# Optimization experiments

Hardware: AMD Instinct MI355X
Metric: run time of the kernel (lower is better)

## Reference

```python
import jax, jax.numpy as jnp
import numpy as np

# Config mirroring MultiHeadAttention1d(in_channels=256, n_heads=8, residual=False,
# kernel_size=1, attention_type=0) applied to 3-D inputs (B, C, N).
B, C, N, H, D = 4, 256, 2048, 8, 256  # per-head dim D = in_channels; OC = H*D = 2048
OC = H * D


def setup_inputs() -> dict:
    key = jax.random.key(0)
    ks = jax.random.split(key, 14)
    s = 1.0 / np.sqrt(C)
    f32 = jnp.float32
    inp = {
        "x": jax.random.normal(ks[0], (B, C, N), f32),
        "y": jax.random.normal(ks[1], (B, C, N), f32),
        # ConvNormActivation1d (kernel_size=1) == pointwise conv + (folded, eval-mode)
        # BatchNorm affine + ReLU. BN folds to per-channel scale g and shift beta.
        "Wq": jax.random.normal(ks[2], (OC, C), f32) * s,
        "bq": jax.random.normal(ks[3], (OC,), f32) * 0.01,
        "gq": jnp.ones((OC,), f32),
        "betaq": jnp.zeros((OC,), f32),
        "Wk": jax.random.normal(ks[4], (OC, C), f32) * s,
        "bk": jax.random.normal(ks[5], (OC,), f32) * 0.01,
        "gk": jnp.ones((OC,), f32),
        "betak": jnp.zeros((OC,), f32),
        "Wv": jax.random.normal(ks[6], (OC, C), f32) * s,
        "bv": jax.random.normal(ks[7], (OC,), f32) * 0.01,
        "gv": jnp.ones((OC,), f32),
        "betav": jnp.zeros((OC,), f32),
    }
    return inp


def _cna(W, b, g, beta, t):
    # 1x1 conv (channel GEMM) + folded-BN affine + ReLU; t: (B, C, N) -> (B, OC, N)
    z = jnp.einsum("oc,bcn->bon", W, t) + b[:, None]
    return jax.nn.relu(g[:, None] * z + beta[:, None])


def _heads(t):
    # (B, OC, N) -> (B, H, N, D); channel split matches torch.split chunks of size D
    return t.reshape(B, H, D, N).transpose(0, 1, 3, 2)


def reference(x, y, Wq, bq, gq, betaq, Wk, bk, gk, betak, Wv, bv, gv, betav):
    q = _heads(_cna(Wq, bq, gq, betaq, x))  # (B,H,N,D)
    k = _heads(_cna(Wk, bk, gk, betak, y))
    v = _heads(_cna(Wv, bv, gv, betav, y))
    energy = jnp.einsum("bhnd,bhmd->bhnm", q, k)  # bmm(Q, K^T)
    attn = jax.nn.softmax(energy, axis=-1)
    out = jnp.einsum("bhnm,bhmd->bhnd", attn, v)  # (B,H,N,D)
    # torch path: view(H,B,k,N,D).permute(1,0,3,2,4) -> (B,H,N,k=1,D);
    # squeeze(dim=2) is a no-op since N != 1.
    return out[:, :, :, None, :]  # (B, H, N, 1, D)
```

## Files before the change

### kernel.cpp

```cpp
#include <hip/hip_runtime.h>
#include <cstdint>
#include <cstddef>

typedef unsigned short u16;
typedef __attribute__((ext_vector_type(4))) float f32x4;
typedef __attribute__((ext_vector_type(16))) float f32x16;
typedef __attribute__((ext_vector_type(8))) _Float16 f16x8;
typedef __attribute__((ext_vector_type(4))) u16   u16x4;
typedef __attribute__((ext_vector_type(8))) u16   u16x8;
typedef __attribute__((ext_vector_type(4))) int   i32x4;

#define DEV static __device__ __forceinline__
#define MFMA16(a,b,c) __builtin_amdgcn_mfma_f32_16x16x32_f16((a),(b),(c),0,0,0)
#define MFMA32(a,b,c) __builtin_amdgcn_mfma_f32_32x32x16_f16((a),(b),(c),0,0,0)

constexpr int Bc = 4, Cc = 256, Nc = 2048, Hc = 8, Dc = 256, OCc = 2048;

constexpr size_t OFF_XT = 0;
constexpr size_t OFF_YT = OFF_XT + (size_t)Bc*Nc*Cc*2;
constexpr size_t OFF_WQ = OFF_YT + (size_t)Bc*Nc*Cc*2;
constexpr size_t OFF_WK = OFF_WQ + (size_t)OCc*Cc*2;
constexpr size_t OFF_WV = OFF_WK + (size_t)OCc*Cc*2;
constexpr size_t OFF_BQ = OFF_WV + (size_t)OCc*Cc*2;
constexpr size_t OFF_BK = OFF_BQ + (size_t)OCc*4;
constexpr size_t OFF_BV = OFF_BK + (size_t)OCc*4;
constexpr size_t OFF_Q  = OFF_BV + (size_t)OCc*4;
constexpr size_t OFF_K  = OFF_Q  + (size_t)Bc*Hc*Nc*Dc*2;
constexpr size_t OFF_V  = OFF_K  + (size_t)Bc*Hc*Nc*Dc*2;

DEV u16 f2h(float x){
  _Float16 h = (_Float16)x;
  return __builtin_bit_cast(u16, h);
}

DEV void load_lds16(const void* g, void* l){
  __builtin_amdgcn_global_load_lds((const __attribute__((address_space(1))) int*)g,
                                   (__attribute__((address_space(3))) int*)l, 16, 0, 0);
}

__global__ __launch_bounds__(256) void transpose_cast(const float* __restrict__ x,
                                                      const float* __restrict__ y,
                                                      u16* __restrict__ XT,
                                                      u16* __restrict__ YT){
  __shared__ u16 tile[64][65];
  int b = blockIdx.z >> 1;
  const float* src = (blockIdx.z & 1) ? y : x;
  u16* dst = (blockIdx.z & 1) ? YT : XT;
  int n0 = blockIdx.x * 64, c0 = blockIdx.y * 64;
  int t = threadIdx.x;
#pragma unroll
  for (int i = 0; i < 16; ++i){
    int slot = i*256 + t;
    int cl = slot >> 6, nl = slot & 63;
    tile[cl][nl] = f2h(src[((size_t)b*Cc + c0 + cl)*Nc + n0 + nl]);
  }
  __syncthreads();
#pragma unroll
  for (int i = 0; i < 8; ++i){
    int slot = i*256 + t;
    int nl = slot >> 5, cl = (slot & 31)*2;
    uint32_t v = (uint32_t)tile[cl][nl] | ((uint32_t)tile[cl+1][nl] << 16);
    *(uint32_t*)(dst + ((size_t)b*Nc + n0 + nl)*Cc + c0 + cl) = v;
  }
}

__global__ __launch_bounds__(256) void prep_w(const float* __restrict__ W,
                                              const float* __restrict__ bsrc,
                                              const float* __restrict__ g,
                                              const float* __restrict__ beta,
                                              u16* __restrict__ Wo,
                                              float* __restrict__ bb){
  int idx = (blockIdx.x*256 + threadIdx.x) * 8;
  int o = idx >> 8, c = idx & 255;
  float gg = g[o];
  f32x4 a0 = *(const f32x4*)(W + idx);
  f32x4 a1 = *(const f32x4*)(W + idx + 4);
  u16x8 r;
#pragma unroll
  for (int i = 0; i < 4; ++i){ r[i] = f2h(a0[i]*gg); r[i+4] = f2h(a1[i]*gg); }
  *(u16x8*)(Wo + idx) = r;
  if (c == 0) bb[o] = gg*bsrc[o] + beta[o];
}

template<int SW>
__global__ __launch_bounds__(256, 2) void proj_gemm(const u16* __restrict__ Xt,
                                                    const u16* __restrict__ Wp,
                                                    const float* __restrict__ bb,
                                                    u16* __restrict__ outp){
  __shared__ __align__(16) char lds[32768];
  int t = threadIdx.x, w = t >> 6, l = t & 63, q = l & 15, g = l >> 4;
  int b = blockIdx.z;
  int n0 = blockIdx.x * 128, o0 = blockIdx.y * 128;
  int fs = ((q >> 1) & 3) << 4;
  int partg = ((l & 3) ^ ((l >> 3) & 3));
  f32x4 acc[4][4] = {};

  for (int it = 0; it < 4; ++it){
    __syncthreads();
#pragma unroll
    for (int j = 0; j < 8; ++j){
      int s = j*4 + w;
      int chunk = s >> 3;
      int off = (s & 7) * 1024;
      int row = (s & 7)*16 + (l >> 2);
      const char* gsrc;
      if (chunk < 2)
        gsrc = (const char*)(Wp + (size_t)(o0 + row)*Cc) + it*128 + chunk*64 + partg*16;
      else
        gsrc = (const char*)(Xt + ((size_t)b*Nc + n0 + row)*Cc) + it*128 + (chunk & 1)*64 + partg*16;
      load_lds16(gsrc, lds + chunk*8192 + off);
    }
    asm volatile("s_waitcnt vmcnt(0)" ::: "memory");
    __syncthreads();
#pragma unroll
    for (int kc = 0; kc < 2; ++kc){
      f16x8 fw[4], fx[4];
#pragma unroll
      for (int i = 0; i < 4; ++i){
        int wrow = (SW ? (w & 1) : (w >> 1))*64 + i*16 + q;
        int xrow = (SW ? (w >> 1) : (w & 1))*64 + i*16 + q;
        fw[i] = *(const f16x8*)(lds + kc*8192 + wrow*64 + ((g*16) ^ fs));
        fx[i] = *(const f16x8*)(lds + 16384 + kc*8192 + xrow*64 + ((g*16) ^ fs));
      }
#pragma unroll
      for (int i = 0; i < 4; ++i)
#pragma unroll
        for (int jj = 0; jj < 4; ++jj){
          if constexpr (!SW) acc[i][jj] = MFMA16(fw[i], fx[jj], acc[i][jj]);
          else               acc[i][jj] = MFMA16(fx[i], fw[jj], acc[i][jj]);
        }
    }
  }

  if constexpr (!SW) {
    f32x4 bias[4];
#pragma unroll
    for (int i = 0; i < 4; ++i) bias[i] = *(const f32x4*)(bb + o0 + (w>>1)*64 + i*16 + 4*g);
#pragma unroll
    for (int i = 0; i < 4; ++i)
#pragma unroll
      for (int jj = 0; jj < 4; ++jj){
        u16x4 pk;
#pragma unroll
        for (int r = 0; r < 4; ++r){
          float z = acc[i][jj][r] + bias[i][r];
          pk[r] = f2h(fmaxf(z, 0.f));
        }
        int o = o0 + (w>>1)*64 + i*16 + 4*g;
        int n = n0 + (w&1)*64 + jj*16 + q;
        int hh = o >> 8, d = o & 255;
        *(u16x4*)(outp + ((size_t)((b*Hc + hh)*Nc + n))*Dc + d) = pk;
      }
  } else {
    float biasv[4];
#pragma unroll
    for (int i = 0; i < 4; ++i) biasv[i] = bb[o0 + (w&1)*64 + i*16 + q];
#pragma unroll
    for (int i = 0; i < 4; ++i)
#pragma unroll
      for (int jj = 0; jj < 4; ++jj){
        u16x4 pk;
#pragma unroll
        for (int r = 0; r < 4; ++r){
          float z = acc[i][jj][r] + biasv[jj];
          pk[r] = f2h(fmaxf(z, 0.f));
        }
        int o = o0 + (w&1)*64 + jj*16 + q;
        int n = n0 + (w>>1)*64 + i*16 + 4*g;
        int hh = o >> 8, d = o & 255;
        *(u16x4*)(outp + ((size_t)((b*Hc + hh)*Dc + d))*Nc + n) = pk;
      }
  }
}

__global__ __launch_bounds__(512, 1) void attn_kernel(const u16* __restrict__ Qp,
                                                      const u16* __restrict__ Kp,
                                                      const u16* __restrict__ Vp,
                                                      float* __restrict__ outp){
  __shared__ __align__(16) char lds[150528];
  const int t = threadIdx.x, w = t >> 6, l = t & 63, lq = l & 31, hi = l >> 5;
  const int wq = w & 3, wm = w >> 2;
  const int h = blockIdx.y, b = blockIdx.z;
  const int q0 = blockIdx.x * 128;
  size_t head = (size_t)(b*Hc + h) * Nc * Dc;
  const u16* Qh = Qp + head;
  const u16* Kh = Kp + head;
  const u16* Vh = Vp + head;

  char* Pex  = lds + 131072;
  float* smax = (float*)(lds + 147456);
  float* ssum = (float*)(lds + 148480);
  float* sscl = (float*)(lds + 149504);
  float* slinv= (float*)(lds + 150016);

  f16x8 qf[16];
  {
    const u16* qrow = Qh + (size_t)(q0 + wq*32 + lq) * Dc;
#pragma unroll
    for (int kc = 0; kc < 16; ++kc) qf[kc] = *(const f16x8*)(qrow + kc*16 + hi*8);
  }

  f32x16 acc[4] = {};
  float m_run = -1e30f, l_run = 0.f;

#define STAGE_KV(m0_, buf_)                                                        \
  {                                                                                \
    char* Kd = lds + (buf_)*32768;                                                 \
    char* Vd = lds + 65536 + (buf_)*32768;                                         \
    _Pragma("unroll")                                                              \
    for (int j = 0; j < 4; ++j){                                                   \
      int row = w*8 + j*2 + hi;                                                    \
      int gs = (l & 31) ^ (row & 7);                                               \
      load_lds16(Kh + (size_t)((m0_) + row)*Dc + gs*8, Kd + w*4096 + j*1024);      \
    }                                                                              \
    _Pragma("unroll")                                                              \
    for (int j = 0; j < 4; ++j){                                                   \
      int ri = w*4 + j;                                                            \
      int rd = ri*8 + (l >> 3);                                                    \
      int gs = (l & 7) ^ (rd & 7);                                                 \
      load_lds16(Vh + (size_t)rd*Nc + (m0_) + gs*8, Vd + ri*1024 + l*16);          \
    }                                                                              \
  }

  STAGE_KV(0, 0);
  asm volatile("s_waitcnt vmcnt(0)" ::: "memory");
  __syncthreads();

  for (int it = 0; it < 32; ++it){
    const int cur = it & 1;
    char* Kc = lds + cur*32768;
    char* Vc = lds + 65536 + cur*32768;

    if (it < 31) STAGE_KV((it + 1)*64, cur ^ 1);

    f32x16 s = {};
    __builtin_amdgcn_s_setprio(1);
#pragma unroll
    for (int kc = 0; kc < 16; ++kc){
      f16x8 kf = *(const f16x8*)(Kc + (wm*32 + lq)*512 + ((kc*32 + hi*16) ^ ((l & 7) << 4)));
      s = MFMA32(kf, qf[kc], s);
    }
    __builtin_amdgcn_s_setprio(0);

    float tmax = s[0];
#pragma unroll
    for (int r = 1; r < 16; ++r) tmax = fmaxf(tmax, s[r]);
    tmax = fmaxf(tmax, __shfl_xor(tmax, 32));
    if (!hi) smax[(wq*2 + wm)*32 + lq] = tmax;
    __syncthreads();
    float omax = smax[(wq*2 + (1 - wm))*32 + lq];
    float mnew = fmaxf(m_run, fmaxf(tmax, omax));
    float scale = __expf(m_run - mnew);

    float p[16];
    float rsum = 0.f;
#pragma unroll
    for (int r = 0; r < 16; ++r){ p[r] = __expf(s[r] - mnew); rsum += p[r]; }
    rsum += __shfl_xor(rsum, 32);
    if (!hi){
      ssum[(wq*2 + wm)*32 + lq] = rsum;
      if (!wm) sscl[wq*32 + lq] = scale;
    }

    int pk[8];
#pragma unroll
    for (int j2 = 0; j2 < 8; ++j2)
      pk[j2] = __builtin_bit_cast(int, __builtin_amdgcn_cvt_pkrtz(p[2*j2], p[2*j2+1]));
    int sx[8];
#pragma unroll
    for (int j2 = 0; j2 < 8; ++j2) sx[j2] = __shfl_xor(pk[j2], 32);
    i32x4 f0, f1;
    f0[0] = hi ? sx[2] : pk[0];  f0[1] = hi ? sx[3] : pk[1];
    f0[2] = hi ? pk[2] : sx[0];  f0[3] = hi ? pk[3] : sx[1];
    f1[0] = hi ? sx[6] : pk[4];  f1[1] = hi ? sx[7] : pk[5];
    f1[2] = hi ? pk[6] : sx[4];  f1[3] = hi ? pk[7] : sx[5];
    *(i32x4*)(Pex + w*2048 + l*16)        = f0;
    *(i32x4*)(Pex + w*2048 + 1024 + l*16) = f1;
    __syncthreads();

    float osum = ssum[(wq*2 + (1 - wm))*32 + lq];
    l_run = l_run * scale + rsum + osum;
    m_run = mnew;

    float sc[16];
#pragma unroll
    for (int r = 0; r < 16; ++r) sc[r] = sscl[wq*32 + (r & 3) + 8*(r >> 2) + 4*hi];
#pragma unroll
    for (int dt = 0; dt < 4; ++dt)
#pragma unroll
      for (int r = 0; r < 16; ++r) acc[dt][r] *= sc[r];

    i32x4 g0 = *(const i32x4*)(Pex + (w ^ 4)*2048 + l*16);
    i32x4 g1 = *(const i32x4*)(Pex + (w ^ 4)*2048 + 1024 + l*16);
    f16x8 a0 = __builtin_bit_cast(f16x8, wm ? g0 : f0);
    f16x8 a1 = __builtin_bit_cast(f16x8, wm ? g1 : f1);
    f16x8 a2 = __builtin_bit_cast(f16x8, wm ? f0 : g0);
    f16x8 a3 = __builtin_bit_cast(f16x8, wm ? f1 : g1);

    __builtin_amdgcn_s_setprio(1);
#pragma unroll
    for (int h2 = 0; h2 < 2; ++h2)
#pragma unroll
      for (int dt = 0; dt < 4; ++dt)
#pragma unroll
        for (int mcl = 0; mcl < 2; ++mcl){
          f16x8 vf = *(const f16x8*)(Vc + (wm*128 + dt*32 + lq)*128 +
                                     (((h2*4 + mcl*2 + hi)*16) ^ ((l & 7) << 4)));
          f16x8 af = h2 ? (mcl ? a3 : a2) : (mcl ? a1 : a0);
          acc[dt] = MFMA32(af, vf, acc[dt]);
        }
    __builtin_amdgcn_s_setprio(0);

    asm volatile("s_waitcnt vmcnt(0)" ::: "memory");
    __syncthreads();
  }
#undef STAGE_KV

  if (!hi && !wm) slinv[wq*32 + lq] = 1.f / l_run;
  __syncthreads();
  float li[16];
#pragma unroll
  for (int r = 0; r < 16; ++r) li[r] = slinv[wq*32 + (r & 3) + 8*(r >> 2) + 4*hi];
#pragma unroll
  for (int dt = 0; dt < 4; ++dt)
#pragma unroll
    for (int r = 0; r < 16; ++r){
      int qrow_ = wq*32 + (r & 3) + 8*(r >> 2) + 4*hi;
      int d = wm*128 + dt*32 + lq;
      outp[head + (size_t)(q0 + qrow_)*Dc + d] = acc[dt][r] * li[r];
    }
}

extern "C" void kernel_launch(void* const* d_in, const int* in_sizes, int n_in,
                              void* d_out, int out_size, void* d_ws, size_t ws_size,
                              hipStream_t stream){
  const float* x     = (const float*)d_in[0];
  const float* y     = (const float*)d_in[1];
  const float* Wq    = (const float*)d_in[2];
  const float* bq    = (const float*)d_in[3];
  const float* gq    = (const float*)d_in[4];
  const float* betaq = (const float*)d_in[5];
  const float* Wk    = (const float*)d_in[6];
  const float* bk    = (const float*)d_in[7];
  const float* gk    = (const float*)d_in[8];
  const float* betak = (const float*)d_in[9];
  const float* Wv    = (const float*)d_in[10];
  const float* bv    = (const float*)d_in[11];
  const float* gv    = (const float*)d_in[12];
  const float* betav = (const float*)d_in[13];
  char* ws = (char*)d_ws;
  float* outp = (float*)d_out;

  u16* XT = (u16*)(ws + OFF_XT);
  u16* YT = (u16*)(ws + OFF_YT);
  u16* WQb = (u16*)(ws + OFF_WQ);
  u16* WKb = (u16*)(ws + OFF_WK);
  u16* WVb = (u16*)(ws + OFF_WV);
  float* BQ = (float*)(ws + OFF_BQ);
  float* BK = (float*)(ws + OFF_BK);
  float* BV = (float*)(ws + OFF_BV);
  u16* Qw = (u16*)(ws + OFF_Q);
  u16* Kw = (u16*)(ws + OFF_K);
  u16* Vw = (u16*)(ws + OFF_V);

  transpose_cast<<<dim3(Nc/64, Cc/64, Bc*2), 256, 0, stream>>>(x, y, XT, YT);
  prep_w<<<dim3(OCc*Cc/2048), 256, 0, stream>>>(Wq, bq, gq, betaq, WQb, BQ);
  prep_w<<<dim3(OCc*Cc/2048), 256, 0, stream>>>(Wk, bk, gk, betak, WKb, BK);
  prep_w<<<dim3(OCc*Cc/2048), 256, 0, stream>>>(Wv, bv, gv, betav, WVb, BV);

  dim3 pg(Nc/128, OCc/128, Bc);
  proj_gemm<0><<<pg, 256, 0, stream>>>(XT, WQb, BQ, Qw);
  proj_gemm<0><<<pg, 256, 0, stream>>>(YT, WKb, BK, Kw);
  proj_gemm<1><<<pg, 256, 0, stream>>>(YT, WVb, BV, Vw);

  attn_kernel<<<dim3(Nc/128, Hc, Bc), 512, 0, stream>>>(Qw, Kw, Vw, outp);
}
```

Baseline: 270.8 us.

## Give each wave full key/value tiles and 32 queries, dropping cross-wave softmax exchange

The attention kernel now processes 256 queries per block, with each of the 8 waves owning 32 query rows and the full 256-wide head dimension and all 64 keys per tile. This removes the shared-memory exchange of row maxima, sums, scales and P fragments and two barriers per iteration. It also adds a lazy rescale that only updates the running max when it grows by more than 8. The cost is doubled accumulator registers (8 f32x16 per lane) and half as many blocks, which risks register spills and fewer blocks to fill the GPU.

```diff
diff --git a/kernel.cpp b/kernel.cpp
--- a/kernel.cpp
+++ b/kernel.cpp
@@ -177,30 +177,23 @@
                                                       const u16* __restrict__ Kp,
                                                       const u16* __restrict__ Vp,
                                                       float* __restrict__ outp){
-  __shared__ __align__(16) char lds[150528];
+  __shared__ __align__(16) char lds[131072];
   const int t = threadIdx.x, w = t >> 6, l = t & 63, lq = l & 31, hi = l >> 5;
-  const int wq = w & 3, wm = w >> 2;
   const int h = blockIdx.y, b = blockIdx.z;
-  const int q0 = blockIdx.x * 128;
+  const int q0 = blockIdx.x * 256;
   size_t head = (size_t)(b*Hc + h) * Nc * Dc;
   const u16* Qh = Qp + head;
   const u16* Kh = Kp + head;
   const u16* Vh = Vp + head;
 
-  char* Pex  = lds + 131072;
-  float* smax = (float*)(lds + 147456);
-  float* ssum = (float*)(lds + 148480);
-  float* sscl = (float*)(lds + 149504);
-  float* slinv= (float*)(lds + 150016);
-
   f16x8 qf[16];
   {
-    const u16* qrow = Qh + (size_t)(q0 + wq*32 + lq) * Dc;
+    const u16* qrow = Qh + (size_t)(q0 + w*32 + lq) * Dc;
 #pragma unroll
     for (int kc = 0; kc < 16; ++kc) qf[kc] = *(const f16x8*)(qrow + kc*16 + hi*8);
   }
 
-  f32x16 acc[4] = {};
+  f32x16 acc[8] = {};
   float m_run = -1e30f, l_run = 0.f;
 
 #define STAGE_KV(m0_, buf_)                                                        \
@@ -218,7 +211,7 @@
       int ri = w*4 + j;                                                            \
       int rd = ri*8 + (l >> 3);                                                    \
       int gs = (l & 7) ^ (rd & 7);                                                 \
-      load_lds16(Vh + (size_t)rd*Nc + (m0_) + gs*8, Vd + ri*1024 + l*16);          \
+      load_lds16(Vh + (size_t)rd*Nc + (m0_) + gs*8, Vd + ri*1024);                 \
     }                                                                              \
   }
 
@@ -233,82 +226,87 @@
 
     if (it < 31) STAGE_KV((it + 1)*64, cur ^ 1);
 
-    f32x16 s = {};
+    f32x16 s0 = {}, s1 = {};
     __builtin_amdgcn_s_setprio(1);
 #pragma unroll
     for (int kc = 0; kc < 16; ++kc){
-      f16x8 kf = *(const f16x8*)(Kc + (wm*32 + lq)*512 + ((kc*32 + hi*16) ^ ((l & 7) << 4)));
-      s = MFMA32(kf, qf[kc], s);
+      int off = (kc*32 + hi*16) ^ ((l & 7) << 4);
+      f16x8 kf0 = *(const f16x8*)(Kc + lq*512 + off);
+      f16x8 kf1 = *(const f16x8*)(Kc + (32 + lq)*512 + off);
+      s0 = MFMA32(kf0, qf[kc], s0);
+      s1 = MFMA32(kf1, qf[kc], s1);
     }
     __builtin_amdgcn_s_setprio(0);
 
-    float tmax = s[0];
-#pragma unroll
-    for (int r = 1; r < 16; ++r) tmax = fmaxf(tmax, s[r]);
+    float tmax = s0[0];
+#pragma unroll
+    for (int r = 1; r < 16; ++r) tmax = fmaxf(tmax, s0[r]);
+#pragma unroll
+    for (int r = 0; r < 16; ++r) tmax = fmaxf(tmax, s1[r]);
     tmax = fmaxf(tmax, __shfl_xor(tmax, 32));
-    if (!hi) smax[(wq*2 + wm)*32 + lq] = tmax;
-    __syncthreads();
-    float omax = smax[(wq*2 + (1 - wm))*32 + lq];
-    float mnew = fmaxf(m_run, fmaxf(tmax, omax));
-    float scale = __expf(m_run - mnew);
-
-    float p[16];
+
+    float meff = m_run, scale = 1.f;
+    if (!__all(tmax <= m_run + 8.f)){
+      meff = fmaxf(m_run, tmax);
+      scale = __expf(m_run - meff);
+      m_run = meff;
+#pragma unroll
+      for (int r = 0; r < 16; ++r){
+        float scr = __shfl(scale, (r & 3) + 8*(r >> 2) + 4*hi);
+#pragma unroll
+        for (int dt = 0; dt < 8; ++dt) acc[dt][r] *= scr;
+      }
+    }
+
     float rsum = 0.f;
 #pragma unroll
-    for (int r = 0; r < 16; ++r){ p[r] = __expf(s[r] - mnew); rsum += p[r]; }
+    for (int r = 0; r < 16; ++r){ s0[r] = __expf(s0[r] - meff); rsum += s0[r]; }
+#pragma unroll
+    for (int r = 0; r < 16; ++r){ s1[r] = __expf(s1[r] - meff); rsum += s1[r]; }
     rsum += __shfl_xor(rsum, 32);
-    if (!hi){
-      ssum[(wq*2 + wm)*32 + lq] = rsum;
-      if (!wm) sscl[wq*32 + lq] = scale;
-    }
-
-    int pk[8];
-#pragma unroll
-    for (int j2 = 0; j2 < 8; ++j2)
-      pk[j2] = __builtin_bit_cast(int, __builtin_amdgcn_cvt_pkrtz(p[2*j2], p[2*j2+1]));
-    int sx[8];
-#pragma unroll
-    for (int j2 = 0; j2 < 8; ++j2) sx[j2] = __shfl_xor(pk[j2], 32);
-    i32x4 f0, f1;
-    f0[0] = hi ? sx[2] : pk[0];  f0[1] = hi ? sx[3] : pk[1];
-    f0[2] = hi ? pk[2] : sx[0];  f0[3] = hi ? pk[3] : sx[1];
-    f1[0] = hi ? sx[6] : pk[4];  f1[1] = hi ? sx[7] : pk[5];
-    f1[2] = hi ? pk[6] : sx[4];  f1[3] = hi ? pk[7] : sx[5];
-    *(i32x4*)(Pex + w*2048 + l*16)        = f0;
-    *(i32x4*)(Pex + w*2048 + 1024 + l*16) = f1;
-    __syncthreads();
-
-    float osum = ssum[(wq*2 + (1 - wm))*32 + lq];
-    l_run = l_run * scale + rsum + osum;
-    m_run = mnew;
-
-    float sc[16];
-#pragma unroll
-    for (int r = 0; r < 16; ++r) sc[r] = sscl[wq*32 + (r & 3) + 8*(r >> 2) + 4*hi];
-#pragma unroll
-    for (int dt = 0; dt < 4; ++dt)
-#pragma unroll
-      for (int r = 0; r < 16; ++r) acc[dt][r] *= sc[r];
-
-    i32x4 g0 = *(const i32x4*)(Pex + (w ^ 4)*2048 + l*16);
-    i32x4 g1 = *(const i32x4*)(Pex + (w ^ 4)*2048 + 1024 + l*16);
-    f16x8 a0 = __builtin_bit_cast(f16x8, wm ? g0 : f0);
-    f16x8 a1 = __builtin_bit_cast(f16x8, wm ? g1 : f1);
-    f16x8 a2 = __builtin_bit_cast(f16x8, wm ? f0 : g0);
-    f16x8 a3 = __builtin_bit_cast(f16x8, wm ? f1 : g1);
+    l_run = l_run * scale + rsum;
+
+    f16x8 a0, a1, a2, a3;
+    {
+      int pk[8], sx[8];
+#pragma unroll
+      for (int j2 = 0; j2 < 8; ++j2)
+        pk[j2] = __builtin_bit_cast(int, __builtin_amdgcn_cvt_pkrtz(s0[2*j2], s0[2*j2+1]));
+#pragma unroll
+      for (int j2 = 0; j2 < 8; ++j2) sx[j2] = __shfl_xor(pk[j2], 32);
+      i32x4 c0, c1;
+      c0[0] = hi ? sx[2] : pk[0];  c0[1] = hi ? sx[3] : pk[1];
+      c0[2] = hi ? pk[2] : sx[0];  c0[3] = hi ? pk[3] : sx[1];
+      c1[0] = hi ? sx[6] : pk[4];  c1[1] = hi ? sx[7] : pk[5];
+      c1[2] = hi ? pk[6] : sx[4];  c1[3] = hi ? pk[7] : sx[5];
+      a0 = __builtin_bit_cast(f16x8, c0);
+      a1 = __builtin_bit_cast(f16x8, c1);
+    }
+    {
+      int pk[8], sx[8];
+#pragma unroll
+      for (int j2 = 0; j2 < 8; ++j2)
+        pk[j2] = __builtin_bit_cast(int, __builtin_amdgcn_cvt_pkrtz(s1[2*j2], s1[2*j2+1]));
+#pragma unroll
+      for (int j2 = 0; j2 < 8; ++j2) sx[j2] = __shfl_xor(pk[j2], 32);
+      i32x4 c0, c1;
+      c0[0] = hi ? sx[2] : pk[0];  c0[1] = hi ? sx[3] : pk[1];
+      c0[2] = hi ? pk[2] : sx[0];  c0[3] = hi ? pk[3] : sx[1];
+      c1[0] = hi ? sx[6] : pk[4];  c1[1] = hi ? sx[7] : pk[5];
+      c1[2] = hi ? pk[6] : sx[4];  c1[3] = hi ? pk[7] : sx[5];
+      a2 = __builtin_bit_cast(f16x8, c0);
+      a3 = __builtin_bit_cast(f16x8, c1);
+    }
 
     __builtin_amdgcn_s_setprio(1);
 #pragma unroll
-    for (int h2 = 0; h2 < 2; ++h2)
-#pragma unroll
-      for (int dt = 0; dt < 4; ++dt)
-#pragma unroll
-        for (int mcl = 0; mcl < 2; ++mcl){
-          f16x8 vf = *(const f16x8*)(Vc + (wm*128 + dt*32 + lq)*128 +
-                                     (((h2*4 + mcl*2 + hi)*16) ^ ((l & 7) << 4)));
-          f16x8 af = h2 ? (mcl ? a3 : a2) : (mcl ? a1 : a0);
-          acc[dt] = MFMA32(af, vf, acc[dt]);
-        }
+    for (int dt = 0; dt < 8; ++dt)
+#pragma unroll
+      for (int ks = 0; ks < 4; ++ks){
+        f16x8 vf = *(const f16x8*)(Vc + (dt*32 + lq)*128 + (((ks*2 + hi) ^ (l & 7)) << 4));
+        f16x8 af = (ks == 0) ? a0 : (ks == 1) ? a1 : (ks == 2) ? a2 : a3;
+        acc[dt] = MFMA32(af, vf, acc[dt]);
+      }
     __builtin_amdgcn_s_setprio(0);
 
     asm volatile("s_waitcnt vmcnt(0)" ::: "memory");
@@ -316,19 +314,16 @@
   }
 #undef STAGE_KV
 
-  if (!hi && !wm) slinv[wq*32 + lq] = 1.f / l_run;
-  __syncthreads();
-  float li[16];
-#pragma unroll
-  for (int r = 0; r < 16; ++r) li[r] = slinv[wq*32 + (r & 3) + 8*(r >> 2) + 4*hi];
-#pragma unroll
-  for (int dt = 0; dt < 4; ++dt)
-#pragma unroll
-    for (int r = 0; r < 16; ++r){
-      int qrow_ = wq*32 + (r & 3) + 8*(r >> 2) + 4*hi;
-      int d = wm*128 + dt*32 + lq;
-      outp[head + (size_t)(q0 + qrow_)*Dc + d] = acc[dt][r] * li[r];
-    }
+  float inv_own = 1.f / l_run;
+#pragma unroll
+  for (int r = 0; r < 16; ++r){
+    int qrow_ = (r & 3) + 8*(r >> 2) + 4*hi;
+    float invr = __shfl(inv_own, (r & 3) + 8*(r >> 2) + 4*hi);
+    size_t obase = head + (size_t)(q0 + w*32 + qrow_)*Dc + lq;
+#pragma unroll
+    for (int dt = 0; dt < 8; ++dt)
+      outp[obase + dt*32] = acc[dt][r] * invr;
+  }
 }
 
 extern "C" void kernel_launch(void* const* d_in, const int* in_sizes, int n_in,
@@ -373,5 +368,5 @@
   proj_gemm<0><<<pg, 256, 0, stream>>>(YT, WKb, BK, Kw);
   proj_gemm<1><<<pg, 256, 0, stream>>>(YT, WVb, BV, Vw);
 
-  attn_kernel<<<dim3(Nc/128, Hc, Bc), 512, 0, stream>>>(Qw, Kw, Vw, outp);
-}
+  attn_kernel<<<dim3(Nc/256, Hc, Bc), 512, 0, stream>>>(Qw, Kw, Vw, outp);
+}
```

New measurement: 629.3 us. 132% more time.

## Load V straight from global into registers, single-buffer K, add lazy softmax rescaling

Applied to the files above, without the earlier changes.

The attention kernel no longer stages V in LDS. Each wave loads its V fragments directly from global memory into registers in two halves, interleaved with the PV MFMAs and with the next K tile prefetch. K becomes single-buffered with a new XOR swizzle, which shrinks LDS from about 150KB to 50KB, and the launch bound is raised to allow several blocks per CU. The softmax now rescales the accumulators only when the running max grows by more than 8, sharing the per-row scale and the inverse sum by shuffle instead of through LDS. This trades LDS capacity for more global traffic and register pressure, and it risks stalls from the uncoalesced strided V reads.

```diff
diff --git a/kernel.cpp b/kernel.cpp
--- a/kernel.cpp
+++ b/kernel.cpp
@@ -173,11 +173,11 @@
   }
 }
 
-__global__ __launch_bounds__(512, 1) void attn_kernel(const u16* __restrict__ Qp,
+__global__ __launch_bounds__(512, 4) void attn_kernel(const u16* __restrict__ Qp,
                                                       const u16* __restrict__ Kp,
                                                       const u16* __restrict__ Vp,
                                                       float* __restrict__ outp){
-  __shared__ __align__(16) char lds[150528];
+  __shared__ __align__(16) char lds[51200];
   const int t = threadIdx.x, w = t >> 6, l = t & 63, lq = l & 31, hi = l >> 5;
   const int wq = w & 3, wm = w >> 2;
   const int h = blockIdx.y, b = blockIdx.z;
@@ -187,11 +187,10 @@
   const u16* Kh = Kp + head;
   const u16* Vh = Vp + head;
 
-  char* Pex  = lds + 131072;
-  float* smax = (float*)(lds + 147456);
-  float* ssum = (float*)(lds + 148480);
-  float* sscl = (float*)(lds + 149504);
-  float* slinv= (float*)(lds + 150016);
+  char* Kl  = lds;
+  char* Pex = lds + 32768;
+  float* smax = (float*)(lds + 49152);
+  float* ssum = (float*)(lds + 50176);
 
   f16x8 qf[16];
   {
@@ -202,42 +201,39 @@
 
   f32x16 acc[4] = {};
   float m_run = -1e30f, l_run = 0.f;
-
-#define STAGE_KV(m0_, buf_)                                                        \
+  const int lsw = lq ^ ((lq >> 3) & 3);
+
+#define STAGE_K(m0_)                                                               \
   {                                                                                \
-    char* Kd = lds + (buf_)*32768;                                                 \
-    char* Vd = lds + 65536 + (buf_)*32768;                                         \
     _Pragma("unroll")                                                              \
     for (int j = 0; j < 4; ++j){                                                   \
       int row = w*8 + j*2 + hi;                                                    \
-      int gs = (l & 31) ^ (row & 7);                                               \
-      load_lds16(Kh + (size_t)((m0_) + row)*Dc + gs*8, Kd + w*4096 + j*1024);      \
+      int r5 = row & 31;                                                           \
+      int gs = (l & 31) ^ r5 ^ ((r5 >> 3) & 3);                                    \
+      load_lds16(Kh + (size_t)((m0_) + row)*Dc + gs*8, Kl + w*4096 + j*1024);      \
     }                                                                              \
-    _Pragma("unroll")                                                              \
-    for (int j = 0; j < 4; ++j){                                                   \
-      int ri = w*4 + j;                                                            \
-      int rd = ri*8 + (l >> 3);                                                    \
-      int gs = (l & 7) ^ (rd & 7);                                                 \
-      load_lds16(Vh + (size_t)rd*Nc + (m0_) + gs*8, Vd + ri*1024 + l*16);          \
-    }                                                                              \
-  }
-
-  STAGE_KV(0, 0);
+  }
+
+  STAGE_K(0);
   asm volatile("s_waitcnt vmcnt(0)" ::: "memory");
   __syncthreads();
 
   for (int it = 0; it < 32; ++it){
-    const int cur = it & 1;
-    char* Kc = lds + cur*32768;
-    char* Vc = lds + 65536 + cur*32768;
-
-    if (it < 31) STAGE_KV((it + 1)*64, cur ^ 1);
+    const int m0 = it * 64;
+    const int mn = ((it < 31) ? (it + 1) : 31) * 64;
+
+    f16x8 vA[8];
+#pragma unroll
+    for (int ks = 0; ks < 2; ++ks)
+#pragma unroll
+      for (int dt = 0; dt < 4; ++dt)
+        vA[ks*4 + dt] = *(const f16x8*)(Vh + (size_t)(wm*128 + dt*32 + lq)*Nc + m0 + ks*16 + hi*8);
 
     f32x16 s = {};
     __builtin_amdgcn_s_setprio(1);
 #pragma unroll
     for (int kc = 0; kc < 16; ++kc){
-      f16x8 kf = *(const f16x8*)(Kc + (wm*32 + lq)*512 + ((kc*32 + hi*16) ^ ((l & 7) << 4)));
+      f16x8 kf = *(const f16x8*)(Kl + (wm*32 + lq)*512 + (((kc*2 + hi) ^ lsw) << 4));
       s = MFMA32(kf, qf[kc], s);
     }
     __builtin_amdgcn_s_setprio(0);
@@ -249,18 +245,27 @@
     if (!hi) smax[(wq*2 + wm)*32 + lq] = tmax;
     __syncthreads();
     float omax = smax[(wq*2 + (1 - wm))*32 + lq];
-    float mnew = fmaxf(m_run, fmaxf(tmax, omax));
-    float scale = __expf(m_run - mnew);
+    float cmax = fmaxf(tmax, omax);
+
+    float meff = m_run, scale = 1.f;
+    if (!__all(cmax <= m_run + 8.f)){
+      meff = fmaxf(m_run, cmax);
+      scale = __expf(m_run - meff);
+      m_run = meff;
+#pragma unroll
+      for (int r = 0; r < 16; ++r){
+        float scr = __shfl(scale, (r & 3) + 8*(r >> 2) + 4*hi);
+#pragma unroll
+        for (int dt = 0; dt < 4; ++dt) acc[dt][r] *= scr;
+      }
+    }
 
     float p[16];
     float rsum = 0.f;
 #pragma unroll
-    for (int r = 0; r < 16; ++r){ p[r] = __expf(s[r] - mnew); rsum += p[r]; }
+    for (int r = 0; r < 16; ++r){ p[r] = __expf(s[r] - meff); rsum += p[r]; }
     rsum += __shfl_xor(rsum, 32);
-    if (!hi){
-      ssum[(wq*2 + wm)*32 + lq] = rsum;
-      if (!wm) sscl[wq*32 + lq] = scale;
-    }
+    if (!hi) ssum[(wq*2 + wm)*32 + lq] = rsum;
 
     int pk[8];
 #pragma unroll
@@ -280,15 +285,6 @@
 
     float osum = ssum[(wq*2 + (1 - wm))*32 + lq];
     l_run = l_run * scale + rsum + osum;
-    m_run = mnew;
-
-    float sc[16];
-#pragma unroll
-    for (int r = 0; r < 16; ++r) sc[r] = sscl[wq*32 + (r & 3) + 8*(r >> 2) + 4*hi];
-#pragma unroll
-    for (int dt = 0; dt < 4; ++dt)
-#pragma unroll
-      for (int r = 0; r < 16; ++r) acc[dt][r] *= sc[r];
 
     i32x4 g0 = *(const i32x4*)(Pex + (w ^ 4)*2048 + l*16);
     i32x4 g1 = *(const i32x4*)(Pex + (w ^ 4)*2048 + 1024 + l*16);
@@ -297,38 +293,49 @@
     f16x8 a2 = __builtin_bit_cast(f16x8, wm ? f0 : g0);
     f16x8 a3 = __builtin_bit_cast(f16x8, wm ? f1 : g1);
 
+    asm volatile("s_waitcnt vmcnt(0)" ::: "memory");
     __builtin_amdgcn_s_setprio(1);
 #pragma unroll
-    for (int h2 = 0; h2 < 2; ++h2)
+    for (int dt = 0; dt < 4; ++dt){
+      acc[dt] = MFMA32(a0, vA[dt],     acc[dt]);
+      acc[dt] = MFMA32(a1, vA[4 + dt], acc[dt]);
+    }
+    __builtin_amdgcn_s_setprio(0);
+
+    f16x8 vB[8];
+#pragma unroll
+    for (int ks = 0; ks < 2; ++ks)
 #pragma unroll
       for (int dt = 0; dt < 4; ++dt)
-#pragma unroll
-        for (int mcl = 0; mcl < 2; ++mcl){
-          f16x8 vf = *(const f16x8*)(Vc + (wm*128 + dt*32 + lq)*128 +
-                                     (((h2*4 + mcl*2 + hi)*16) ^ ((l & 7) << 4)));
-          f16x8 af = h2 ? (mcl ? a3 : a2) : (mcl ? a1 : a0);
-          acc[dt] = MFMA32(af, vf, acc[dt]);
-        }
+        vB[ks*4 + dt] = *(const f16x8*)(Vh + (size_t)(wm*128 + dt*32 + lq)*Nc + m0 + 32 + ks*16 + hi*8);
+
+    STAGE_K(mn);
+
+    asm volatile("s_waitcnt vmcnt(4)" ::: "memory");
+
+    __builtin_amdgcn_s_setprio(1);
+#pragma unroll
+    for (int dt = 0; dt < 4; ++dt){
+      acc[dt] = MFMA32(a2, vB[dt],     acc[dt]);
+      acc[dt] = MFMA32(a3, vB[4 + dt], acc[dt]);
+    }
     __builtin_amdgcn_s_setprio(0);
 
     asm volatile("s_waitcnt vmcnt(0)" ::: "memory");
     __syncthreads();
   }
-#undef STAGE_KV
-
-  if (!hi && !wm) slinv[wq*32 + lq] = 1.f / l_run;
-  __syncthreads();
-  float li[16];
-#pragma unroll
-  for (int r = 0; r < 16; ++r) li[r] = slinv[wq*32 + (r & 3) + 8*(r >> 2) + 4*hi];
-#pragma unroll
-  for (int dt = 0; dt < 4; ++dt)
-#pragma unroll
-    for (int r = 0; r < 16; ++r){
-      int qrow_ = wq*32 + (r & 3) + 8*(r >> 2) + 4*hi;
-      int d = wm*128 + dt*32 + lq;
-      outp[head + (size_t)(q0 + qrow_)*Dc + d] = acc[dt][r] * li[r];
-    }
+#undef STAGE_K
+
+  float inv_own = 1.f / l_run;
+#pragma unroll
+  for (int r = 0; r < 16; ++r){
+    int crow = (r & 3) + 8*(r >> 2) + 4*hi;
+    float invr = __shfl(inv_own, crow);
+    size_t obase = head + (size_t)(q0 + wq*32 + crow)*Dc + wm*128 + lq;
+#pragma unroll
+    for (int dt = 0; dt < 4; ++dt)
+      outp[obase + dt*32] = acc[dt][r] * invr;
+  }
 }
 
 extern "C" void kernel_launch(void* const* d_in, const int* in_sizes, int n_in,
```

New measurement: 1.020 ms. 3.77x slower.

## Skip softmax rescale when max grows little, retune LDS swizzle, shuffle scales

Applied to the files above, without the earlier changes.

Adds a lazy online-softmax update: the running max and the accumulator rescale are only refreshed when some row's new max exceeds the running max by more than a threshold, checked wave-wide. Per-row scale and final 1/l are broadcast with lane shuffles instead of LDS round trips. The K tile swizzle gains an extra XOR term to cut LDS bank conflicts on reads. The V LDS destination offset drops the per-lane term, presumably because the LDS DMA load addresses per lane implicitly. The lazy max trades fewer exp and multiply passes for some risk of fp16 P overflow or precision loss if the threshold is too loose.

```diff
diff --git a/kernel.cpp b/kernel.cpp
--- a/kernel.cpp
+++ b/kernel.cpp
@@ -190,8 +190,6 @@
   char* Pex  = lds + 131072;
   float* smax = (float*)(lds + 147456);
   float* ssum = (float*)(lds + 148480);
-  float* sscl = (float*)(lds + 149504);
-  float* slinv= (float*)(lds + 150016);
 
   f16x8 qf[16];
   {
@@ -202,6 +200,7 @@
 
   f32x16 acc[4] = {};
   float m_run = -1e30f, l_run = 0.f;
+  const int lsw = lq ^ ((lq >> 3) & 3);
 
 #define STAGE_KV(m0_, buf_)                                                        \
   {                                                                                \
@@ -210,7 +209,8 @@
     _Pragma("unroll")                                                              \
     for (int j = 0; j < 4; ++j){                                                   \
       int row = w*8 + j*2 + hi;                                                    \
-      int gs = (l & 31) ^ (row & 7);                                               \
+      int r5 = row & 31;                                                           \
+      int gs = (l & 31) ^ r5 ^ ((r5 >> 3) & 3);                                    \
       load_lds16(Kh + (size_t)((m0_) + row)*Dc + gs*8, Kd + w*4096 + j*1024);      \
     }                                                                              \
     _Pragma("unroll")                                                              \
@@ -218,7 +218,7 @@
       int ri = w*4 + j;                                                            \
       int rd = ri*8 + (l >> 3);                                                    \
       int gs = (l & 7) ^ (rd & 7);                                                 \
-      load_lds16(Vh + (size_t)rd*Nc + (m0_) + gs*8, Vd + ri*1024 + l*16);          \
+      load_lds16(Vh + (size_t)rd*Nc + (m0_) + gs*8, Vd + ri*1024);                 \
     }                                                                              \
   }
 
@@ -237,7 +237,7 @@
     __builtin_amdgcn_s_setprio(1);
 #pragma unroll
     for (int kc = 0; kc < 16; ++kc){
-      f16x8 kf = *(const f16x8*)(Kc + (wm*32 + lq)*512 + ((kc*32 + hi*16) ^ ((l & 7) << 4)));
+      f16x8 kf = *(const f16x8*)(Kc + (wm*32 + lq)*512 + (((kc*2 + hi) ^ lsw) << 4));
       s = MFMA32(kf, qf[kc], s);
     }
     __builtin_amdgcn_s_setprio(0);
@@ -249,18 +249,22 @@
     if (!hi) smax[(wq*2 + wm)*32 + lq] = tmax;
     __syncthreads();
     float omax = smax[(wq*2 + (1 - wm))*32 + lq];
-    float mnew = fmaxf(m_run, fmaxf(tmax, omax));
-    float scale = __expf(m_run - mnew);
+    float cmax = fmaxf(tmax, omax);
+
+    float meff = m_run, scale = 1.f;
+    const bool need = !__all(cmax <= m_run + 8.f);
+    if (need){
+      meff = fmaxf(m_run, cmax);
+      scale = __expf(m_run - meff);
+      m_run = meff;
+    }
 
     float p[16];
     float rsum = 0.f;
 #pragma unroll
-    for (int r = 0; r < 16; ++r){ p[r] = __expf(s[r] - mnew); rsum += p[r]; }
+    for (int r = 0; r < 16; ++r){ p[r] = __expf(s[r] - meff); rsum += p[r]; }
     rsum += __shfl_xor(rsum, 32);
-    if (!hi){
-      ssum[(wq*2 + wm)*32 + lq] = rsum;
-      if (!wm) sscl[wq*32 + lq] = scale;
-    }
+    if (!hi) ssum[(wq*2 + wm)*32 + lq] = rsum;
 
     int pk[8];
 #pragma unroll
@@ -280,15 +284,15 @@
 
     float osum = ssum[(wq*2 + (1 - wm))*32 + lq];
     l_run = l_run * scale + rsum + osum;
-    m_run = mnew;
-
-    float sc[16];
-#pragma unroll
-    for (int r = 0; r < 16; ++r) sc[r] = sscl[wq*32 + (r & 3) + 8*(r >> 2) + 4*hi];
-#pragma unroll
-    for (int dt = 0; dt < 4; ++dt)
-#pragma unroll
-      for (int r = 0; r < 16; ++r) acc[dt][r] *= sc[r];
+
+    if (need){
+#pragma unroll
+      for (int r = 0; r < 16; ++r){
+        float scr = __shfl(scale, (r & 3) + 8*(r >> 2) + 4*hi);
+#pragma unroll
+        for (int dt = 0; dt < 4; ++dt) acc[dt][r] *= scr;
+      }
+    }
 
     i32x4 g0 = *(const i32x4*)(Pex + (w ^ 4)*2048 + l*16);
     i32x4 g1 = *(const i32x4*)(Pex + (w ^ 4)*2048 + 1024 + l*16);
@@ -316,19 +320,16 @@
   }
 #undef STAGE_KV
 
-  if (!hi && !wm) slinv[wq*32 + lq] = 1.f / l_run;
-  __syncthreads();
-  float li[16];
-#pragma unroll
-  for (int r = 0; r < 16; ++r) li[r] = slinv[wq*32 + (r & 3) + 8*(r >> 2) + 4*hi];
-#pragma unroll
-  for (int dt = 0; dt < 4; ++dt)
-#pragma unroll
-    for (int r = 0; r < 16; ++r){
-      int qrow_ = wq*32 + (r & 3) + 8*(r >> 2) + 4*hi;
-      int d = wm*128 + dt*32 + lq;
-      outp[head + (size_t)(q0 + qrow_)*Dc + d] = acc[dt][r] * li[r];
-    }
+  float inv_own = 1.f / l_run;
+#pragma unroll
+  for (int r = 0; r < 16; ++r){
+    int crow = (r & 3) + 8*(r >> 2) + 4*hi;
+    float invr = __shfl(inv_own, crow);
+    size_t obase = head + (size_t)(q0 + wq*32 + crow)*Dc + wm*128 + lq;
+#pragma unroll
+    for (int dt = 0; dt < 4; ++dt)
+      outp[obase + dt*32] = acc[dt][r] * invr;
+  }
 }
 
 extern "C" void kernel_launch(void* const* d_in, const int* in_sizes, int n_in,
```

Measured after the change: 267.7 us. Within noise of the previous version (-1.2%).
